# Optimization experiments

Hardware: AMD Instinct MI355X
Metric: run time of the kernel (lower is better)

## Reference

```python
import jax, jax.numpy as jnp
import numpy as np

N = 100000      # nodes
E = 1600000     # edges (before self-loops)
IN = 256        # in_channels
H = 4           # heads (layer 1)
C = 16          # hidden_channels
OUT = 40        # out_channels
NEG_SLOPE = 0.2  # PyG GATConv default


def setup_inputs() -> dict:
    key = jax.random.key(0)
    ks = jax.random.split(key, 10)
    x = jax.random.normal(ks[0], (N, IN), dtype=jnp.float32)
    edge_index = jax.random.randint(ks[1], (2, E), 0, N, dtype=jnp.int64)
    s = 0.1
    return {
        "x": x,
        "edge_index": edge_index,
        "W1": jax.random.normal(ks[2], (IN, H * C), dtype=jnp.float32) * s,
        "a_src1": jax.random.normal(ks[3], (H, C), dtype=jnp.float32) * s,
        "a_dst1": jax.random.normal(ks[4], (H, C), dtype=jnp.float32) * s,
        "b1": jnp.zeros((H * C,), dtype=jnp.float32),
        "W2": jax.random.normal(ks[5], (H * C, OUT), dtype=jnp.float32) * s,
        "a_src2": jax.random.normal(ks[6], (1, OUT), dtype=jnp.float32) * s,
        "a_dst2": jax.random.normal(ks[7], (1, OUT), dtype=jnp.float32) * s,
        "b2": jnp.zeros((OUT,), dtype=jnp.float32),
    }


def gat_conv(x, src, dst, W, a_s, a_d, b, heads, ch, n):
    # x: [n, d_in] -> projected [n, heads, ch]
    xp = (x @ W).reshape(n, heads, ch)
    # per-node attention contributions [n, heads]
    e_s = jnp.einsum('nhc,hc->nh', xp, a_s)
    e_d = jnp.einsum('nhc,hc->nh', xp, a_d)
    # per-edge logits (gather) [E, heads]
    e = jax.nn.leaky_relu(e_s[src] + e_d[dst], negative_slope=NEG_SLOPE)
    # segment softmax over edges sharing a destination node
    m = jax.ops.segment_max(e, dst, num_segments=n)
    m = jnp.where(jnp.isfinite(m), m, 0.0)
    ex = jnp.exp(e - m[dst])
    z = jax.ops.segment_sum(ex, dst, num_segments=n)
    alpha = ex / (z[dst] + 1e-16)               # [E, heads]
    # weighted scatter-add aggregation [n, heads, ch]
    out = jax.ops.segment_sum(xp[src] * alpha[:, :, None], dst, num_segments=n)
    return out.reshape(n, heads * ch) + b       # concat heads + bias


def reference(x, edge_index, W1, a_src1, a_dst1, b1, W2, a_src2, a_dst2, b2):
    n = x.shape[0]
    loop = jnp.arange(n, dtype=edge_index.dtype)
    src = jnp.concatenate([edge_index[0], loop])  # PyG add_self_loops=True
    dst = jnp.concatenate([edge_index[1], loop])
    h = gat_conv(x, src, dst, W1, a_src1, a_dst1, b1, H, C, n)
    h = jax.nn.relu(h)
    out = gat_conv(h, src, dst, W2, a_src2, a_dst2, b2, 1, OUT, n)
    return out
```

## Files before the change

### kernel.cpp

```cpp
#include <hip/hip_runtime.h>
#include <hip/hip_bf16.h>

#define IN_DIM 256
#define HC     64
#define OUT_DIM 40
#define NEG    0.2f

#define NB_SH   8
#define NB_MASK 255
#define SRC_BITS 17
#define SRC_MASK 0x1FFFF
#define CHUNK   8192
#define LEN_CAP 6144

typedef __bf16 bf16x8 __attribute__((ext_vector_type(8)));
typedef float  f32x4  __attribute__((ext_vector_type(4)));

__device__ inline float lrelu(float v) { return fmaxf(v, NEG * v); }

__global__ __launch_bounds__(256) void hist_kernel(
    const int* __restrict__ ei, int* __restrict__ blkhist, int E, int ET, int nbuck) {
  __shared__ int hist[512];
  int tid = threadIdx.x;
  for (int i = tid; i < nbuck; i += 256) hist[i] = 0;
  __syncthreads();
  int base = blockIdx.x * CHUNK;
  #pragma unroll 4
  for (int it = 0; it < CHUNK / 256; ++it) {
    int e = base + it * 256 + tid;
    if (e < ET) {
      int d = (e < E) ? ei[E + e] : (e - E);
      atomicAdd(&hist[d >> NB_SH], 1);
    }
  }
  __syncthreads();
  for (int i = tid; i < nbuck; i += 256) blkhist[blockIdx.x * nbuck + i] = hist[i];
}

__global__ __launch_bounds__(256) void bsum_kernel(
    const int* __restrict__ blkhist, int* __restrict__ btot, int nblk, int nbuck) {
  __shared__ int sm[256];
  int b = blockIdx.x, tid = threadIdx.x;
  int s = 0;
  for (int i = tid; i < nblk; i += 256) s += blkhist[(size_t)i * nbuck + b];
  sm[tid] = s; __syncthreads();
  #pragma unroll
  for (int o = 128; o; o >>= 1) {
    if (tid < o) sm[tid] += sm[tid + o];
    __syncthreads();
  }
  if (tid == 0) btot[b] = sm[0];
}

__global__ __launch_bounds__(512) void bscan_kernel(
    const int* __restrict__ btot, int* __restrict__ bstart,
    int* __restrict__ offs, int nbuck, int ET, int n) {
  __shared__ int sm[512];
  int tid = threadIdx.x;
  int total = (tid < nbuck) ? btot[tid] : 0;
  sm[tid] = total; __syncthreads();
  for (int o = 1; o < 512; o <<= 1) {
    int v = (tid >= o) ? sm[tid - o] : 0;
    __syncthreads();
    sm[tid] += v;
    __syncthreads();
  }
  if (tid < nbuck) bstart[tid] = sm[tid] - total;
  if (tid == 0) { bstart[nbuck] = ET; offs[n] = ET; }
}

__global__ __launch_bounds__(256) void curs_kernel(
    const int* __restrict__ blkhist, const int* __restrict__ bstart,
    int* __restrict__ cur, int nblk, int nbuck) {
  __shared__ int sm[256];
  int b = blockIdx.x, tid = threadIdx.x;
  int run = bstart[b];
  for (int c = 0; c < nblk; c += 256) {
    int idx = c + tid;
    int v = (idx < nblk) ? blkhist[(size_t)idx * nbuck + b] : 0;
    sm[tid] = v; __syncthreads();
    for (int o = 1; o < 256; o <<= 1) {
      int x = (tid >= o) ? sm[tid - o] : 0;
      __syncthreads();
      sm[tid] += x;
      __syncthreads();
    }
    if (idx < nblk) cur[(size_t)idx * nbuck + b] = run + sm[tid] - v;
    run += sm[255];
    __syncthreads();
  }
}

__global__ __launch_bounds__(512) void scatter1_kernel(
    const int* __restrict__ ei, const int* __restrict__ cur,
    unsigned int* __restrict__ pairs, int E, int ET, int nbuck) {
  __shared__ int hs[512];
  __shared__ int addb[512];
  __shared__ int lcnt[512];
  __shared__ unsigned int lout[CHUNK];
  __shared__ int ldst[CHUNK];
  int tid = threadIdx.x, blk = blockIdx.x, base = blk * CHUNK;
  hs[tid] = 0; lcnt[tid] = 0;
  __syncthreads();
  #pragma unroll 4
  for (int it = 0; it < CHUNK / 512; ++it) {
    int e = base + it * 512 + tid;
    if (e < ET) {
      int d = (e < E) ? ei[E + e] : (e - E);
      atomicAdd(&hs[d >> NB_SH], 1);
    }
  }
  __syncthreads();
  int t = hs[tid];
  for (int o = 1; o < 512; o <<= 1) {
    int v = (tid >= o) ? hs[tid - o] : 0;
    __syncthreads();
    hs[tid] += v;
    __syncthreads();
  }
  int lofs = hs[tid] - t;
  __syncthreads();
  hs[tid] = lofs;
  addb[tid] = ((tid < nbuck) ? cur[(size_t)blk * nbuck + tid] : 0) - lofs;
  __syncthreads();
  #pragma unroll 4
  for (int it = 0; it < CHUNK / 512; ++it) {
    int e = base + it * 512 + tid;
    if (e < ET) {
      int s, d;
      if (e < E) { s = ei[e]; d = ei[E + e]; }
      else       { s = e - E; d = s; }
      int b = d >> NB_SH;
      int pos = hs[b] + atomicAdd(&lcnt[b], 1);
      lout[pos] = (unsigned)s | ((unsigned)(d & NB_MASK) << SRC_BITS);
      ldst[pos] = addb[b] + pos;
    }
  }
  __syncthreads();
  int len = min(CHUNK, ET - base);
  for (int i = tid; i < len; i += 512) pairs[ldst[i]] = lout[i];
}

__global__ __launch_bounds__(512) void place2_kernel(
    const unsigned int* __restrict__ pairs, const int* __restrict__ bstart,
    int* __restrict__ offs, int* __restrict__ srcs, int n, int nbuck) {
  __shared__ unsigned int lin[LEN_CAP];
  __shared__ unsigned int lou[LEN_CAP];
  __shared__ int lhs[256];
  __shared__ int lcnt[256];
  __shared__ int sm[512];
  int b = blockIdx.x, tid = threadIdx.x;
  int rbeg = bstart[b], rend = bstart[b + 1], len = rend - rbeg;
  int node0 = b << NB_SH;
  int nloc = min(256, n - node0);
  if (tid < 256) { lhs[tid] = 0; lcnt[tid] = 0; }
  __syncthreads();
  if (len <= LEN_CAP) {
    for (int i = tid; i < len; i += 512) {
      unsigned p = pairs[rbeg + i];
      lin[i] = p;
      atomicAdd(&lhs[(p >> SRC_BITS) & NB_MASK], 1);
    }
    __syncthreads();
    int t = (tid < 256) ? lhs[tid] : 0;
    sm[tid] = t; __syncthreads();
    for (int o = 1; o < 512; o <<= 1) {
      int v = (tid >= o) ? sm[tid - o] : 0;
      __syncthreads();
      sm[tid] += v;
      __syncthreads();
    }
    int excl = sm[tid] - t;
    if (tid < nloc) offs[node0 + tid] = rbeg + excl;
    if (tid < 256) lhs[tid] = excl;
    __syncthreads();
    for (int i = tid; i < len; i += 512) {
      unsigned p = lin[i];
      int dl = (p >> SRC_BITS) & NB_MASK;
      int pos = lhs[dl] + atomicAdd(&lcnt[dl], 1);
      lou[pos] = p & SRC_MASK;
    }
    __syncthreads();
    for (int i = tid; i < len; i += 512) srcs[rbeg + i] = (int)lou[i];
  } else {
    for (int i = tid; i < len; i += 512)
      atomicAdd(&lhs[(pairs[rbeg + i] >> SRC_BITS) & NB_MASK], 1);
    __syncthreads();
    int t = (tid < 256) ? lhs[tid] : 0;
    sm[tid] = t; __syncthreads();
    for (int o = 1; o < 512; o <<= 1) {
      int v = (tid >= o) ? sm[tid - o] : 0;
      __syncthreads();
      sm[tid] += v;
      __syncthreads();
    }
    int excl = sm[tid] - t;
    if (tid < nloc) offs[node0 + tid] = rbeg + excl;
    if (tid < 256) lhs[tid] = excl;
    __syncthreads();
    for (int i = tid; i < len; i += 512) {
      unsigned p = pairs[rbeg + i];
      int dl = (p >> SRC_BITS) & NB_MASK;
      int pos = lhs[dl] + atomicAdd(&lcnt[dl], 1);
      srcs[rbeg + pos] = (int)(p & SRC_MASK);
    }
  }
}

__global__ void wprep_kernel(const float* __restrict__ W1, __bf16* __restrict__ Wt) {
  int i = blockIdx.x * blockDim.x + threadIdx.x;
  if (i >= IN_DIM * HC) return;
  int k = i >> 6, nn = i & 63;
  Wt[nn * IN_DIM + k] = (__bf16)W1[i];
}

__global__ __launch_bounds__(256) void gemm1_mfma(
    const float* __restrict__ x, const __bf16* __restrict__ Wt,
    const float* __restrict__ a_s, const float* __restrict__ a_d,
    __bf16* __restrict__ xp1b, float* __restrict__ es1, float* __restrict__ ed1, int n) {
  __shared__ uint4 wl[2048];
  int tid = threadIdx.x;
  const uint4* gw = (const uint4*)Wt;
  #pragma unroll
  for (int it = 0; it < 8; ++it) {
    int c16 = it * 256 + tid;
    int row = c16 >> 5;
    int swz = c16 ^ (row & 7);
    wl[swz] = gw[c16];
  }
  __syncthreads();

  int wave = tid >> 6, lane = tid & 63;
  int l15 = lane & 15, kgrp = lane >> 4;
  int rowA = blockIdx.x * 64 + wave * 16 + l15;
  bool okA = rowA < n;
  const float* xrow = x + (size_t)(okA ? rowA : (n - 1)) * IN_DIM;

  f32x4 va[8][2];
  #pragma unroll
  for (int c = 0; c < 8; ++c) {
    int k0 = c * 32 + kgrp * 8;
    va[c][0] = *(const f32x4*)(xrow + k0);
    va[c][1] = *(const f32x4*)(xrow + k0 + 4);
  }
  __builtin_amdgcn_sched_barrier(0);
  asm volatile("" : "+v"(va[0][0]), "+v"(va[0][1]), "+v"(va[1][0]), "+v"(va[1][1]),
                    "+v"(va[2][0]), "+v"(va[2][1]), "+v"(va[3][0]), "+v"(va[3][1]),
                    "+v"(va[4][0]), "+v"(va[4][1]), "+v"(va[5][0]), "+v"(va[5][1]),
                    "+v"(va[6][0]), "+v"(va[6][1]), "+v"(va[7][0]), "+v"(va[7][1]));

  f32x4 acc[4] = {};
  #pragma unroll
  for (int c = 0; c < 8; ++c) {
    bf16x8 ahi, alo;
    #pragma unroll
    for (int i = 0; i < 4; ++i) {
      float f0 = va[c][0][i], f1 = va[c][1][i];
      __bf16 h0 = (__bf16)f0, h1 = (__bf16)f1;
      ahi[i]     = h0;
      ahi[4 + i] = h1;
      alo[i]     = (__bf16)(f0 - (float)h0);
      alo[4 + i] = (__bf16)(f1 - (float)h1);
    }
    #pragma unroll
    for (int t = 0; t < 4; ++t) {
      int row  = t * 16 + l15;
      int unit = row * 32 + c * 4 + kgrp;
      int swz  = unit ^ (row & 7);
      bf16x8 b = *(const bf16x8*)&wl[swz];
      acc[t] = __builtin_amdgcn_mfma_f32_16x16x32_bf16(ahi, b, acc[t], 0, 0, 0);
      acc[t] = __builtin_amdgcn_mfma_f32_16x16x32_bf16(alo, b, acc[t], 0, 0, 0);
    }
  }

  int rowbase = blockIdx.x * 64 + wave * 16 + kgrp * 4;
  #pragma unroll
  for (int t = 0; t < 4; ++t) {
    float as_v = a_s[t * 16 + l15], ad_v = a_d[t * 16 + l15];
    #pragma unroll
    for (int r = 0; r < 4; ++r) {
      int row = rowbase + r;
      float v = acc[t][r];
      bool ok = row < n;
      if (ok) xp1b[(size_t)row * HC + t * 16 + l15] = (__bf16)v;
      float ps = v * as_v, pd = v * ad_v;
      #pragma unroll
      for (int o = 1; o < 16; o <<= 1) {
        ps += __shfl_xor(ps, o, 16);
        pd += __shfl_xor(pd, o, 16);
      }
      if (ok && l15 == 0) {
        es1[row * 4 + t] = ps;
        ed1[row * 4 + t] = pd;
      }
    }
  }
}

__global__ __launch_bounds__(256) void agg1_csr(
    const int* __restrict__ offs, const int* __restrict__ srcs,
    const float* __restrict__ es1, const float* __restrict__ ed1,
    const __bf16* __restrict__ xp1b, const float* __restrict__ b1,
    float* __restrict__ hout, int n) {
  __shared__ float lds[4][16 * 4 * 2];
  int wave = threadIdx.x >> 6;
  int wid = (blockIdx.x * 256 + threadIdx.x) >> 6;
  if (wid >= n) return;
  int lane = threadIdx.x & 63;
  int eidx = lane >> 2, hA = lane & 3;
  int a = lane & 31, half = lane >> 5;
  int ch0 = a * 2, headB = a >> 3;
  int beg = offs[wid], end = offs[wid + 1];
  float edh = ed1[wid * 4 + hA];
  float zacc = 0.f, acc0 = 0.f, acc1 = 0.f;
  const char* xbase = (const char*)xp1b + ch0 * 2;
  float* myl = lds[wave];

  for (int e0 = beg; e0 < end; e0 += 16) {
    int cnt = min(16, end - e0);
    float ex = 0.f;
    int s = 0;
    if (eidx < cnt) {
      s = srcs[e0 + eidx];
      ex = __expf(lrelu(es1[s * 4 + hA] + edh));
    }
    zacc += ex;
    myl[lane * 2]     = ex;
    myl[lane * 2 + 1] = __int_as_float(s * (int)(HC * sizeof(__bf16)));
    if (cnt == 16) {
      float2 ao[8];
      #pragma unroll
      for (int jp = 0; jp < 8; ++jp)
        ao[jp] = *(const float2*)&myl[((jp * 2 + half) * 4 + headB) * 2];
      unsigned wj[8];
      #pragma unroll
      for (int jp = 0; jp < 8; ++jp)
        wj[jp] = *(const unsigned*)(xbase + __float_as_int(ao[jp].y));
      #pragma unroll
      for (int jp = 0; jp < 8; ++jp) {
        float f0 = __int_as_float((int)(wj[jp] << 16));
        float f1 = __int_as_float((int)(wj[jp] & 0xffff0000u));
        acc0 = fmaf(ao[jp].x, f0, acc0);
        acc1 = fmaf(ao[jp].x, f1, acc1);
      }
    } else {
      int jpmax = (cnt + 1 - half) >> 1;
      #pragma unroll 4
      for (int jp = 0; jp < jpmax; ++jp) {
        float2 ao = *(const float2*)&myl[((jp * 2 + half) * 4 + headB) * 2];
        unsigned w = *(const unsigned*)(xbase + __float_as_int(ao.y));
        float f0 = __int_as_float((int)(w << 16));
        float f1 = __int_as_float((int)(w & 0xffff0000u));
        acc0 = fmaf(ao.x, f0, acc0);
        acc1 = fmaf(ao.x, f1, acc1);
      }
    }
  }

  float z = zacc;
  z += __shfl_xor(z, 4); z += __shfl_xor(z, 8);
  z += __shfl_xor(z, 16); z += __shfl_xor(z, 32);
  float zc = __shfl(z, headB);
  acc0 += __shfl_xor(acc0, 32);
  acc1 += __shfl_xor(acc1, 32);
  if (half == 0) {
    float inv = 1.f / (zc + 1e-16f);
    float2 r;
    r.x = fmaxf(fmaf(acc0, inv, b1[ch0]), 0.f);
    r.y = fmaxf(fmaf(acc1, inv, b1[ch0 + 1]), 0.f);
    *(float2*)&hout[(size_t)wid * HC + ch0] = r;
  }
}

__global__ __launch_bounds__(256) void layer2_mfma(
    const float* __restrict__ h, const float* __restrict__ W2,
    const float* __restrict__ a_s2, const float* __restrict__ a_d2,
    __bf16* __restrict__ xp2b, float* __restrict__ es2, float* __restrict__ ed2, int n) {
  int tid = threadIdx.x;
  int wave = tid >> 6, lane = tid & 63;
  int l15 = lane & 15, kgrp = lane >> 4;
  int rowA = blockIdx.x * 64 + wave * 16 + l15;
  const float* hrow = h + (size_t)(rowA < n ? rowA : (n - 1)) * HC;

  f32x4 va[2][2];
  #pragma unroll
  for (int c = 0; c < 2; ++c) {
    int k0 = c * 32 + kgrp * 8;
    va[c][0] = *(const f32x4*)(hrow + k0);
    va[c][1] = *(const f32x4*)(hrow + k0 + 4);
  }
  bf16x8 ahi[2], alo[2];
  #pragma unroll
  for (int c = 0; c < 2; ++c) {
    #pragma unroll
    for (int i = 0; i < 4; ++i) {
      float f0 = va[c][0][i], f1 = va[c][1][i];
      __bf16 h0 = (__bf16)f0, h1 = (__bf16)f1;
      ahi[c][i]     = h0;
      ahi[c][4 + i] = h1;
      alo[c][i]     = (__bf16)(f0 - (float)h0);
      alo[c][4 + i] = (__bf16)(f1 - (float)h1);
    }
  }

  f32x4 acc[3] = {};
  #pragma unroll
  for (int c = 0; c < 2; ++c) {
    #pragma unroll
    for (int t = 0; t < 3; ++t) {
      int col = t * 16 + l15;
      bool okc = col < OUT_DIM;
      bf16x8 bhi, blo;
      #pragma unroll
      for (int i = 0; i < 8; ++i) {
        int k = c * 32 + kgrp * 8 + i;
        float w = okc ? W2[k * OUT_DIM + col] : 0.f;
        __bf16 wh = (__bf16)w;
        bhi[i] = wh;
        blo[i] = (__bf16)(w - (float)wh);
      }
      acc[t] = __builtin_amdgcn_mfma_f32_16x16x32_bf16(ahi[c], bhi, acc[t], 0, 0, 0);
      acc[t] = __builtin_amdgcn_mfma_f32_16x16x32_bf16(ahi[c], blo, acc[t], 0, 0, 0);
      acc[t] = __builtin_amdgcn_mfma_f32_16x16x32_bf16(alo[c], bhi, acc[t], 0, 0, 0);
    }
  }

  int rowbase = blockIdx.x * 64 + wave * 16 + kgrp * 4;
  #pragma unroll
  for (int r = 0; r < 4; ++r) {
    int row = rowbase + r;
    bool ok = row < n;
    float ps = 0.f, pd = 0.f;
    #pragma unroll
    for (int t = 0; t < 3; ++t) {
      int col = t * 16 + l15;
      if (col < OUT_DIM) {
        float v = acc[t][r];
        if (ok) xp2b[(size_t)row * OUT_DIM + col] = (__bf16)v;
        ps = fmaf(v, a_s2[col], ps);
        pd = fmaf(v, a_d2[col], pd);
      }
    }
    #pragma unroll
    for (int o = 1; o < 16; o <<= 1) {
      ps += __shfl_xor(ps, o, 16);
      pd += __shfl_xor(pd, o, 16);
    }
    if (ok && l15 == 0) { es2[row] = ps; ed2[row] = pd; }
  }
}

__global__ __launch_bounds__(256) void agg2_csr(
    const int* __restrict__ offs, const int* __restrict__ srcs,
    const float* __restrict__ es2, const float* __restrict__ ed2,
    const __bf16* __restrict__ xp2b, const float* __restrict__ b2,
    float* __restrict__ out, int n) {
  __shared__ float lds[4][64 * 2];
  int wave = threadIdx.x >> 6;
  int wid = (blockIdx.x * 256 + threadIdx.x) >> 6;
  if (wid >= n) return;
  int lane = threadIdx.x & 63;
  int beg = offs[wid], end = offs[wid + 1];
  float edv = ed2[wid];
  float zacc = 0.f, acc = 0.f;
  const char* xcol = (const char*)(xp2b + lane);
  float* myl = lds[wave];

  for (int e0 = beg; e0 < end; e0 += 64) {
    int cnt = min(64, end - e0);
    float ex = 0.f;
    int s = 0;
    if (lane < cnt) {
      s = srcs[e0 + lane];
      ex = __expf(lrelu(es2[s] + edv));
    }
    zacc += ex;
    myl[lane * 2]     = ex;
    myl[lane * 2 + 1] = __int_as_float(s * (int)(OUT_DIM * sizeof(__bf16)));
    if (lane < OUT_DIM) {
      int jb = 0;
      for (; jb + 8 <= cnt; jb += 8) {
        float2 ao[8];
        #pragma unroll
        for (int k = 0; k < 8; ++k) ao[k] = *(const float2*)&myl[(jb + k) * 2];
        float xv[8];
        #pragma unroll
        for (int k = 0; k < 8; ++k)
          xv[k] = (float)*(const __bf16*)(xcol + __float_as_int(ao[k].y));
        #pragma unroll
        for (int k = 0; k < 8; ++k) acc = fmaf(ao[k].x, xv[k], acc);
      }
      #pragma unroll 4
      for (; jb < cnt; ++jb) {
        float2 ao = *(const float2*)&myl[jb * 2];
        float xv = (float)*(const __bf16*)(xcol + __float_as_int(ao.y));
        acc = fmaf(ao.x, xv, acc);
      }
    }
  }

  float z = zacc;
  #pragma unroll
  for (int o = 1; o < 64; o <<= 1) z += __shfl_xor(z, o);
  if (lane < OUT_DIM)
    out[(size_t)wid * OUT_DIM + lane] = acc / (z + 1e-16f) + b2[lane];
}

extern "C" void kernel_launch(void* const* d_in, const int* in_sizes, int n_in,
                              void* d_out, int out_size, void* d_ws, size_t ws_size,
                              hipStream_t stream) {
  const float* x    = (const float*)d_in[0];
  const int*   ei   = (const int*)d_in[1];
  const float* W1   = (const float*)d_in[2];
  const float* a_s1 = (const float*)d_in[3];
  const float* a_d1 = (const float*)d_in[4];
  const float* b1   = (const float*)d_in[5];
  const float* W2   = (const float*)d_in[6];
  const float* a_s2 = (const float*)d_in[7];
  const float* a_d2 = (const float*)d_in[8];
  const float* b2   = (const float*)d_in[9];

  int n  = in_sizes[0] / IN_DIM;
  int E  = in_sizes[1] / 2;
  int ET = E + n;
  int nbuck = (n + 255) >> NB_SH;
  int nblk1 = (ET + CHUNK - 1) / CHUNK;
  float* out = (float*)d_out;

  char* ws = (char*)d_ws;
  size_t off = 0;
  auto alloc = [&](size_t bytes) -> void* {
    void* p = ws + off;
    off = (off + bytes + 255) & ~(size_t)255;
    return p;
  };
  __bf16* xp1b    = (__bf16*)alloc((size_t)n * HC * 2);
  __bf16* xp2b    = (__bf16*)alloc((size_t)n * OUT_DIM * 2);
  float*  h       = (float*)alloc((size_t)n * HC * 4);
  float*  es1     = (float*)alloc((size_t)n * 4 * 4);
  float*  ed1     = (float*)alloc((size_t)n * 4 * 4);
  float*  es2     = (float*)alloc((size_t)n * 4);
  float*  ed2     = (float*)alloc((size_t)n * 4);
  int*    blkhist = (int*)alloc((size_t)nblk1 * nbuck * 4);
  int*    cur     = (int*)alloc((size_t)nblk1 * nbuck * 4);
  int*    btot    = (int*)alloc((size_t)(nbuck + 1) * 4);
  int*    bstart  = (int*)alloc((size_t)(nbuck + 1) * 4);
  int*    offs    = (int*)alloc((size_t)(n + 1) * 4);
  int*    srcs    = (int*)alloc((size_t)ET * 4);
  unsigned int* pairs = (unsigned int*)alloc((size_t)ET * 4);
  __bf16* Wt      = (__bf16*)alloc((size_t)IN_DIM * HC * 2);

  hist_kernel<<<nblk1, 256, 0, stream>>>(ei, blkhist, E, ET, nbuck);
  bsum_kernel<<<nbuck, 256, 0, stream>>>(blkhist, btot, nblk1, nbuck);
  bscan_kernel<<<1, 512, 0, stream>>>(btot, bstart, offs, nbuck, ET, n);
  curs_kernel<<<nbuck, 256, 0, stream>>>(blkhist, bstart, cur, nblk1, nbuck);
  scatter1_kernel<<<nblk1, 512, 0, stream>>>(ei, cur, pairs, E, ET, nbuck);
  place2_kernel<<<nbuck, 512, 0, stream>>>(pairs, bstart, offs, srcs, n, nbuck);

  wprep_kernel<<<(IN_DIM * HC + 255) / 256, 256, 0, stream>>>(W1, Wt);
  gemm1_mfma<<<(n + 63) / 64, 256, 0, stream>>>(x, Wt, a_s1, a_d1,
                                                xp1b, es1, ed1, n);
  agg1_csr<<<(n * 64 + 255) / 256, 256, 0, stream>>>(offs, srcs, es1, ed1, xp1b, b1, h, n);
  layer2_mfma<<<(n + 63) / 64, 256, 0, stream>>>(h, W2, a_s2, a_d2, xp2b, es2, ed2, n);
  agg2_csr<<<(n * 64 + 255) / 256, 256, 0, stream>>>(offs, srcs, es2, ed2, xp2b, b2, out, n);
}
```

Baseline: 204.6 us.

## Make layer-1 GEMM persistent with double-buffered prefetch of x tiles

Replaces the one-tile-per-block layer-1 projection GEMM with a persistent kernel of 512 blocks that loop over 64-row tiles. Each block keeps two register buffers filled by inline-asm global loads, so the next tile's x rows are fetched while the current tile runs through MFMA. The W tile is loaded into LDS once per block and reused across tiles instead of once per tile. The cost is higher register pressure from two 16-vector buffers, which may lower occupancy. The full vmcnt(0) wait also drains stores issued by the previous iteration.

```diff
diff --git a/kernel.cpp b/kernel.cpp
--- a/kernel.cpp
+++ b/kernel.cpp
@@ -214,10 +214,81 @@
   Wt[nn * IN_DIM + k] = (__bf16)W1[i];
 }
 
-__global__ __launch_bounds__(256) void gemm1_mfma(
+
+#define GL16(P, A) asm volatile( \
+  "global_load_dwordx4 %[o0], %[p], off\n\t" \
+  "global_load_dwordx4 %[o1], %[p], off offset:16\n\t" \
+  "global_load_dwordx4 %[o2], %[p], off offset:128\n\t" \
+  "global_load_dwordx4 %[o3], %[p], off offset:144\n\t" \
+  "global_load_dwordx4 %[o4], %[p], off offset:256\n\t" \
+  "global_load_dwordx4 %[o5], %[p], off offset:272\n\t" \
+  "global_load_dwordx4 %[o6], %[p], off offset:384\n\t" \
+  "global_load_dwordx4 %[o7], %[p], off offset:400\n\t" \
+  "global_load_dwordx4 %[o8], %[p], off offset:512\n\t" \
+  "global_load_dwordx4 %[o9], %[p], off offset:528\n\t" \
+  "global_load_dwordx4 %[oa], %[p], off offset:640\n\t" \
+  "global_load_dwordx4 %[ob], %[p], off offset:656\n\t" \
+  "global_load_dwordx4 %[oc], %[p], off offset:768\n\t" \
+  "global_load_dwordx4 %[od], %[p], off offset:784\n\t" \
+  "global_load_dwordx4 %[oe], %[p], off offset:896\n\t" \
+  "global_load_dwordx4 %[of], %[p], off offset:912" \
+  : [o0]"=&v"(A[0]),  [o1]"=&v"(A[1]),  [o2]"=&v"(A[2]),  [o3]"=&v"(A[3]), \
+    [o4]"=&v"(A[4]),  [o5]"=&v"(A[5]),  [o6]"=&v"(A[6]),  [o7]"=&v"(A[7]), \
+    [o8]"=&v"(A[8]),  [o9]"=&v"(A[9]),  [oa]"=&v"(A[10]), [ob]"=&v"(A[11]), \
+    [oc]"=&v"(A[12]), [od]"=&v"(A[13]), [oe]"=&v"(A[14]), [of]"=&v"(A[15]) \
+  : [p]"v"(P) : "memory")
+
+#define WAITV() do { asm volatile("s_waitcnt vmcnt(0)" ::: "memory"); \
+                     __builtin_amdgcn_sched_barrier(0); } while (0)
+
+#define COMPUTE_STORE(A, TILE) do { \
+  f32x4 acc[4] = {}; \
+  _Pragma("unroll") \
+  for (int c = 0; c < 8; ++c) { \
+    bf16x8 ahi, alo; \
+    _Pragma("unroll") \
+    for (int i = 0; i < 4; ++i) { \
+      float f0 = A[c * 2][i], f1 = A[c * 2 + 1][i]; \
+      __bf16 h0 = (__bf16)f0, h1 = (__bf16)f1; \
+      ahi[i] = h0; ahi[4 + i] = h1; \
+      alo[i] = (__bf16)(f0 - (float)h0); alo[4 + i] = (__bf16)(f1 - (float)h1); \
+    } \
+    _Pragma("unroll") \
+    for (int t = 0; t < 4; ++t) { \
+      int row  = t * 16 + l15; \
+      int unit = row * 32 + c * 4 + kgrp; \
+      int swz  = unit ^ (row & 7); \
+      bf16x8 bb = *(const bf16x8*)&wl[swz]; \
+      acc[t] = __builtin_amdgcn_mfma_f32_16x16x32_bf16(ahi, bb, acc[t], 0, 0, 0); \
+      acc[t] = __builtin_amdgcn_mfma_f32_16x16x32_bf16(alo, bb, acc[t], 0, 0, 0); \
+    } \
+  } \
+  int rowbase = (TILE) * 64 + wave * 16 + kgrp * 4; \
+  _Pragma("unroll") \
+  for (int t = 0; t < 4; ++t) { \
+    float as_v = a_s[t * 16 + l15], ad_v = a_d[t * 16 + l15]; \
+    _Pragma("unroll") \
+    for (int r = 0; r < 4; ++r) { \
+      int row = rowbase + r; \
+      float v = acc[t][r]; \
+      bool ok = row < n; \
+      if (ok) xp1b[(size_t)row * HC + t * 16 + l15] = (__bf16)v; \
+      float ps = v * as_v, pd = v * ad_v; \
+      _Pragma("unroll") \
+      for (int o = 1; o < 16; o <<= 1) { \
+        ps += __shfl_xor(ps, o, 16); \
+        pd += __shfl_xor(pd, o, 16); \
+      } \
+      if (ok && l15 == 0) { es1[row * 4 + t] = ps; ed1[row * 4 + t] = pd; } \
+    } \
+  } \
+} while (0)
+
+__global__ __launch_bounds__(256) void gemm1_v3(
     const float* __restrict__ x, const __bf16* __restrict__ Wt,
     const float* __restrict__ a_s, const float* __restrict__ a_d,
-    __bf16* __restrict__ xp1b, float* __restrict__ es1, float* __restrict__ ed1, int n) {
+    __bf16* __restrict__ xp1b, float* __restrict__ es1, float* __restrict__ ed1,
+    int n, int ntiles) {
   __shared__ uint4 wl[2048];
   int tid = threadIdx.x;
   const uint4* gw = (const uint4*)Wt;
@@ -232,68 +303,32 @@
 
   int wave = tid >> 6, lane = tid & 63;
   int l15 = lane & 15, kgrp = lane >> 4;
-  int rowA = blockIdx.x * 64 + wave * 16 + l15;
-  bool okA = rowA < n;
-  const float* xrow = x + (size_t)(okA ? rowA : (n - 1)) * IN_DIM;
-
-  f32x4 va[8][2];
-  #pragma unroll
-  for (int c = 0; c < 8; ++c) {
-    int k0 = c * 32 + kgrp * 8;
-    va[c][0] = *(const f32x4*)(xrow + k0);
-    va[c][1] = *(const f32x4*)(xrow + k0 + 4);
-  }
-  __builtin_amdgcn_sched_barrier(0);
-  asm volatile("" : "+v"(va[0][0]), "+v"(va[0][1]), "+v"(va[1][0]), "+v"(va[1][1]),
-                    "+v"(va[2][0]), "+v"(va[2][1]), "+v"(va[3][0]), "+v"(va[3][1]),
-                    "+v"(va[4][0]), "+v"(va[4][1]), "+v"(va[5][0]), "+v"(va[5][1]),
-                    "+v"(va[6][0]), "+v"(va[6][1]), "+v"(va[7][0]), "+v"(va[7][1]));
-
-  f32x4 acc[4] = {};
-  #pragma unroll
-  for (int c = 0; c < 8; ++c) {
-    bf16x8 ahi, alo;
-    #pragma unroll
-    for (int i = 0; i < 4; ++i) {
-      float f0 = va[c][0][i], f1 = va[c][1][i];
-      __bf16 h0 = (__bf16)f0, h1 = (__bf16)f1;
-      ahi[i]     = h0;
-      ahi[4 + i] = h1;
-      alo[i]     = (__bf16)(f0 - (float)h0);
-      alo[4 + i] = (__bf16)(f1 - (float)h1);
-    }
-    #pragma unroll
-    for (int t = 0; t < 4; ++t) {
-      int row  = t * 16 + l15;
-      int unit = row * 32 + c * 4 + kgrp;
-      int swz  = unit ^ (row & 7);
-      bf16x8 b = *(const bf16x8*)&wl[swz];
-      acc[t] = __builtin_amdgcn_mfma_f32_16x16x32_bf16(ahi, b, acc[t], 0, 0, 0);
-      acc[t] = __builtin_amdgcn_mfma_f32_16x16x32_bf16(alo, b, acc[t], 0, 0, 0);
-    }
-  }
-
-  int rowbase = blockIdx.x * 64 + wave * 16 + kgrp * 4;
-  #pragma unroll
-  for (int t = 0; t < 4; ++t) {
-    float as_v = a_s[t * 16 + l15], ad_v = a_d[t * 16 + l15];
-    #pragma unroll
-    for (int r = 0; r < 4; ++r) {
-      int row = rowbase + r;
-      float v = acc[t][r];
-      bool ok = row < n;
-      if (ok) xp1b[(size_t)row * HC + t * 16 + l15] = (__bf16)v;
-      float ps = v * as_v, pd = v * ad_v;
-      #pragma unroll
-      for (int o = 1; o < 16; o <<= 1) {
-        ps += __shfl_xor(ps, o, 16);
-        pd += __shfl_xor(pd, o, 16);
-      }
-      if (ok && l15 == 0) {
-        es1[row * 4 + t] = ps;
-        ed1[row * 4 + t] = pd;
-      }
-    }
+
+  auto aptr = [&](int tile) -> const float* {
+    int rowA = tile * 64 + wave * 16 + l15;
+    if (rowA >= n) rowA = n - 1;
+    return x + (size_t)rowA * IN_DIM + kgrp * 8;
+  };
+
+  f32x4 bufA[16], bufB[16];
+  int tile = blockIdx.x;
+  if (tile >= ntiles) return;
+  const int stride = gridDim.x;
+
+  GL16(aptr(tile), bufA);
+  while (true) {
+    int nt = tile + stride;
+    WAITV();
+    if (nt < ntiles) GL16(aptr(nt), bufB);
+    COMPUTE_STORE(bufA, tile);
+    if (nt >= ntiles) break;
+    tile = nt;
+    nt = tile + stride;
+    WAITV();
+    if (nt < ntiles) GL16(aptr(nt), bufA);
+    COMPUTE_STORE(bufB, tile);
+    if (nt >= ntiles) break;
+    tile = nt;
   }
 }
 
@@ -525,6 +560,7 @@
   int ET = E + n;
   int nbuck = (n + 255) >> NB_SH;
   int nblk1 = (ET + CHUNK - 1) / CHUNK;
+  int ntiles = (n + 63) / 64;
   float* out = (float*)d_out;
 
   char* ws = (char*)d_ws;
@@ -558,8 +594,7 @@
   place2_kernel<<<nbuck, 512, 0, stream>>>(pairs, bstart, offs, srcs, n, nbuck);
 
   wprep_kernel<<<(IN_DIM * HC + 255) / 256, 256, 0, stream>>>(W1, Wt);
-  gemm1_mfma<<<(n + 63) / 64, 256, 0, stream>>>(x, Wt, a_s1, a_d1,
-                                                xp1b, es1, ed1, n);
+  gemm1_v3<<<512, 256, 0, stream>>>(x, Wt, a_s1, a_d1, xp1b, es1, ed1, n, ntiles);
   agg1_csr<<<(n * 64 + 255) / 256, 256, 0, stream>>>(offs, srcs, es1, ed1, xp1b, b1, h, n);
   layer2_mfma<<<(n + 63) / 64, 256, 0, stream>>>(h, W2, a_s2, a_d2, xp2b, es2, ed2, n);
   agg2_csr<<<(n * 64 + 255) / 256, 256, 0, stream>>>(offs, srcs, es2, ed2, xp2b, b2, out, n);
```

New measurement: 207.8 us. About the same (+1.6%).
